# Optimization experiments

Hardware: AMD Instinct MI355X
Metric: run time of the kernel (lower is better)

The kernel has to match this reference:

```python
import jax, jax.numpy as jnp
import numpy as np

N_USER = 27094
M_SPOT = 42852
N_EDGE = 2_000_000
D_FEAT = 128


def setup_inputs() -> dict:
    key = jax.random.key(0)
    k1, k2, k3, k4 = jax.random.split(key, 4)
    spot_x = jax.random.normal(k1, (M_SPOT, D_FEAT), dtype=jnp.float32)
    user_x = jax.random.normal(k2, (N_USER, D_FEAT), dtype=jnp.float32)
    u_idx = jax.random.randint(k3, (N_EDGE,), 0, N_USER, dtype=jnp.int32)
    s_idx = jax.random.randint(k4, (N_EDGE,), 0, M_SPOT, dtype=jnp.int32)
    user_spot = jnp.stack([u_idx, s_idx], axis=0)  # [2, E]
    return {"spot_x": spot_x, "user_x": user_x, "user_spot": user_spot}


def reference(spot_x, user_x, user_spot):
    u = user_spot[0]  # [E] user index per edge
    s = user_spot[1]  # [E] spot index per edge
    # symmetric GCN normalization: 1/sqrt(deg_u * deg_s) per edge
    user_deg = jnp.bincount(u, length=N_USER)
    spot_deg = jnp.bincount(s, length=M_SPOT)
    div = jnp.sqrt((user_deg[u] * spot_deg[s]).astype(spot_x.dtype))[:, None]  # [E,1]
    # spot -> user aggregation
    source_spot = spot_x[s] / div                                   # [E, D]
    user_out = jax.ops.segment_sum(source_spot, u, num_segments=N_USER)
    # user -> spot aggregation
    source_user = user_x[u] / div                                   # [E, D]
    spot_out = jax.ops.segment_sum(source_user, s, num_segments=M_SPOT)
    return (spot_out, user_out)
```

## Files before the change

kernel.cpp:

```cpp
#include <hip/hip_runtime.h>
#include <stdint.h>


#define NPB_LOG2 6
#define NPB 64
#define MAXB 768
#define PART_CHUNK 2048
#define BH_CHUNK 16384
#define SORT_CAP 8192
#define CSCAN_CH 256

__device__ __forceinline__ ushort f2bf(float f) {
    uint32_t u = __float_as_uint(f);
    return (ushort)((u + 0x7fffu + ((u >> 16) & 1u)) >> 16);
}

__global__ __launch_bounds__(256) void bhist_kernel(
        const int* __restrict__ u, const int* __restrict__ s, int E,
        int nbu, int nbs, int* __restrict__ bd) {
    __shared__ int hist[2 * MAXB];
    const int tid = threadIdx.x;
    const int nb = nbu + nbs;
    const int beg = blockIdx.x * BH_CHUNK;
    const int end = min(beg + BH_CHUNK, E);
    for (int b = tid; b < nb; b += 256) hist[b] = 0;
    __syncthreads();
    for (int i = beg + tid; i < end; i += 256) {
        atomicAdd(&hist[u[i] >> NPB_LOG2], 1);
        atomicAdd(&hist[nbu + (s[i] >> NPB_LOG2)], 1);
    }
    __syncthreads();
    for (int b = tid; b < nb; b += 256) {
        int h = hist[b];
        if (h) atomicAdd(&bd[b], h);
    }
}

__global__ __launch_bounds__(1024) void scan2_kernel(
        const int* __restrict__ bd, int nbu, int nbs,
        int* __restrict__ buoff, int* __restrict__ bsoff,
        int* __restrict__ gcu, int* __restrict__ gcs) {
    __shared__ int wsums[16];
    __shared__ int total;
    const int tid = threadIdx.x, lane = tid & 63, wid = tid >> 6;
    const int n   = blockIdx.x ? nbs : nbu;
    const int* in = blockIdx.x ? (bd + nbu) : bd;
    int* out = blockIdx.x ? bsoff : buoff;
    int* gc  = blockIdx.x ? gcs   : gcu;
    int v = (tid < n) ? in[tid] : 0;
    int x = v;
#pragma unroll
    for (int d = 1; d < 64; d <<= 1) {
        int t = __shfl_up(x, d);
        if (lane >= d) x += t;
    }
    if (lane == 63) wsums[wid] = x;
    __syncthreads();
    if (tid == 0) {
        int run = 0;
#pragma unroll
        for (int w = 0; w < 16; ++w) { int t = wsums[w]; wsums[w] = run; run += t; }
        total = run;
    }
    __syncthreads();
    int excl = wsums[wid] + (x - v);
    if (tid < n) { out[tid] = excl; gc[tid] = excl; }
    if (tid == 0) out[n] = total;
}

__global__ void convert_kernel(const float* __restrict__ x, const float* __restrict__ isd,
                               ushort* __restrict__ xb, int n_rows) {
    int idx = blockIdx.x * blockDim.x + threadIdx.x;
    if (idx >= (n_rows << 6)) return;
    int row = idx >> 6, c = idx & 63;
    float w = isd[row];
    const float* xr = x + ((size_t)row << 7);
    ushort2 o;
    o.x = f2bf(xr[c] * w);
    o.y = f2bf(xr[c + 64] * w);
    *reinterpret_cast<ushort2*>(xb + ((size_t)row << 7) + 2 * c) = o;
}

__global__ __launch_bounds__(256) void part_kernel(
        const int* __restrict__ prim, const int* __restrict__ sec, int E,
        int nb, int* __restrict__ gcur, uint32_t* __restrict__ out) {
    __shared__ int hist[MAXB];
    __shared__ int loff[MAXB];
    __shared__ int gbase[MAXB];
    __shared__ int cur[MAXB];
    __shared__ int wsum[4];
    __shared__ uint32_t sbuf[PART_CHUNK];
    const int tid = threadIdx.x;
    const int lane = tid & 63;
    const int wid = tid >> 6;
    const int beg = blockIdx.x * PART_CHUNK;
    const int end = min(beg + PART_CHUNK, E);
    const int cnt_total = end - beg;
    for (int b = tid; b < nb; b += 256) hist[b] = 0;
    __syncthreads();
    for (int i = beg + tid; i < end; i += 256)
        atomicAdd(&hist[prim[i] >> NPB_LOG2], 1);
    __syncthreads();
    {
        int b0 = tid * 3;
        int h0 = (b0 + 0 < nb) ? hist[b0 + 0] : 0;
        int h1 = (b0 + 1 < nb) ? hist[b0 + 1] : 0;
        int h2 = (b0 + 2 < nb) ? hist[b0 + 2] : 0;
        int tsum = h0 + h1 + h2;
        int x = tsum;
#pragma unroll
        for (int d = 1; d < 64; d <<= 1) {
            int t = __shfl_up(x, d);
            if (lane >= d) x += t;
        }
        if (lane == 63) wsum[wid] = x;
        __syncthreads();
        if (tid == 0) {
            int run = 0;
#pragma unroll
            for (int w = 0; w < 4; ++w) { int t = wsum[w]; wsum[w] = run; run += t; }
        }
        __syncthreads();
        int base = wsum[wid] + (x - tsum);
        if (b0 + 0 < nb) loff[b0 + 0] = base;
        if (b0 + 1 < nb) loff[b0 + 1] = base + h0;
        if (b0 + 2 < nb) loff[b0 + 2] = base + h0 + h1;
    }
    __syncthreads();
    for (int b = tid; b < nb; b += 256) {
        cur[b] = loff[b];
        int c = hist[b];
        gbase[b] = c > 0 ? atomicAdd(&gcur[b], c) : 0;
    }
    __syncthreads();
    for (int i = beg + tid; i < end; i += 256) {
        int p = prim[i], s = sec[i];
        int b = p >> NPB_LOG2;
        int l = atomicAdd(&cur[b], 1);
        sbuf[l] = ((uint32_t)p << 16) | (uint32_t)s;
    }
    __syncthreads();
    for (int k = tid; k < cnt_total; k += 256) {
        uint32_t p = sbuf[k];
        int b = (int)(p >> (16 + NPB_LOG2));
        out[gbase[b] + (k - loff[b])] = p;
    }
}

__global__ __launch_bounds__(256) void bsort3_kernel(
        uint32_t* __restrict__ buf, const int* __restrict__ boff,
        float* __restrict__ isd, int n_rows) {
    __shared__ uint32_t stage[SORT_CAP];
    __shared__ int hist[NPB];
    __shared__ int cur[NPB];
    const int tid = threadIdx.x;
    const int jbeg = boff[blockIdx.x];
    const int cnt = boff[blockIdx.x + 1] - jbeg;
    const bool fits = (cnt <= SORT_CAP);
    if (tid < NPB) hist[tid] = 0;
    __syncthreads();
    for (int k = tid; k < cnt; k += 256) {
        uint32_t p = buf[jbeg + k];
        if (fits) stage[k] = p;
        atomicAdd(&hist[(p >> 16) & (NPB - 1)], 1);
    }
    __syncthreads();
    if (tid < NPB) {
        int h = hist[tid];
        int x = h;
#pragma unroll
        for (int d = 1; d < 64; d <<= 1) {
            int t = __shfl_up(x, d);
            if (tid >= d) x += t;
        }
        cur[tid] = x - h;
        int node = (blockIdx.x << NPB_LOG2) + tid;
        if (node < n_rows) isd[node] = h > 0 ? rsqrtf((float)h) : 0.f;
    }
    __syncthreads();
    if (fits) {
        for (int k = tid; k < cnt; k += 256) {
            uint32_t p = stage[k];
            int slot = atomicAdd(&cur[(p >> 16) & (NPB - 1)], 1);
            buf[jbeg + slot] = p;
        }
    }
}

__global__ __launch_bounds__(256) void cscan_kernel(
        const ushort* __restrict__ xb, const uint32_t* __restrict__ packed, int E,
        const float* __restrict__ isd, float* __restrict__ out) {
    const int lane = threadIdx.x & 63;
    const int wave = (blockIdx.x << 2) + (threadIdx.x >> 6);
    const int base = wave * CSCAN_CH;
    if (base >= E) return;
    const int n = min(CSCAN_CH, E - base);
    const uint32_t* pp = packed + base;
    float ax = 0.f, ay = 0.f;
    int cur = (int)(pp[0] >> 16);

#define ROW(pv) (*reinterpret_cast<const uint32_t*>( \
        xb + (((size_t)((pv) & 0xffffu)) << 7) + (lane << 1)))
#define UPX(rv) __uint_as_float((rv) << 16)
#define UPY(rv) __uint_as_float((rv) & 0xffff0000u)
#define FLUSH() do { float w_ = isd[cur];                                  \
        unsafeAtomicAdd(out + ((size_t)cur << 7) + lane, ax * w_);         \
        unsafeAtomicAdd(out + ((size_t)cur << 7) + 64 + lane, ay * w_);    \
        ax = 0.f; ay = 0.f; } while (0)
#define PROC(pv, rv) do { int d_ = (int)((pv) >> 16);                      \
        if (d_ != cur) { FLUSH(); cur = d_; }                              \
        ax += UPX(rv); ay += UPY(rv); } while (0)
#define GRP8(Aa, Ab, r0, r1, r2, r3, r4, r5, r6, r7) do {                  \
    if ((((Aa.x ^ Ab.w) >> 16) == 0) && ((int)(Aa.x >> 16) == cur)) {      \
        float sx = ((UPX(r0) + UPX(r1)) + (UPX(r2) + UPX(r3)))             \
                 + ((UPX(r4) + UPX(r5)) + (UPX(r6) + UPX(r7)));            \
        float sy = ((UPY(r0) + UPY(r1)) + (UPY(r2) + UPY(r3)))             \
                 + ((UPY(r4) + UPY(r5)) + (UPY(r6) + UPY(r7)));            \
        ax += sx; ay += sy;                                                \
    } else {                                                               \
        PROC(Aa.x, r0); PROC(Aa.y, r1); PROC(Aa.z, r2); PROC(Aa.w, r3);    \
        PROC(Ab.x, r4); PROC(Ab.y, r5); PROC(Ab.z, r6); PROC(Ab.w, r7);    \
    } } while (0)

    int k = 0;
    if (n >= 24) {
        uint4 P0a = *(const uint4*)(pp + 0),  P0b = *(const uint4*)(pp + 4);
        uint4 P1a = *(const uint4*)(pp + 8),  P1b = *(const uint4*)(pp + 12);
        uint32_t a0 = ROW(P0a.x), a1 = ROW(P0a.y), a2 = ROW(P0a.z), a3 = ROW(P0a.w),
                 a4 = ROW(P0b.x), a5 = ROW(P0b.y), a6 = ROW(P0b.z), a7 = ROW(P0b.w);
        uint4 P2a = *(const uint4*)(pp + 16), P2b = *(const uint4*)(pp + 20);
        uint32_t b0 = ROW(P1a.x), b1 = ROW(P1a.y), b2 = ROW(P1a.z), b3 = ROW(P1a.w),
                 b4 = ROW(P1b.x), b5 = ROW(P1b.y), b6 = ROW(P1b.z), b7 = ROW(P1b.w);
        for (k = 24; k + 8 <= n; k += 8) {
            uint4 P3a = *(const uint4*)(pp + k), P3b = *(const uint4*)(pp + k + 4);
            uint32_t c0 = ROW(P2a.x), c1 = ROW(P2a.y), c2 = ROW(P2a.z), c3 = ROW(P2a.w),
                     c4 = ROW(P2b.x), c5 = ROW(P2b.y), c6 = ROW(P2b.z), c7 = ROW(P2b.w);
            GRP8(P0a, P0b, a0, a1, a2, a3, a4, a5, a6, a7);
            P0a = P1a; P0b = P1b; P1a = P2a; P1b = P2b; P2a = P3a; P2b = P3b;
            a0 = b0; a1 = b1; a2 = b2; a3 = b3; a4 = b4; a5 = b5; a6 = b6; a7 = b7;
            b0 = c0; b1 = c1; b2 = c2; b3 = c3; b4 = c4; b5 = c5; b6 = c6; b7 = c7;
        }
        uint32_t c0 = ROW(P2a.x), c1 = ROW(P2a.y), c2 = ROW(P2a.z), c3 = ROW(P2a.w),
                 c4 = ROW(P2b.x), c5 = ROW(P2b.y), c6 = ROW(P2b.z), c7 = ROW(P2b.w);
        GRP8(P0a, P0b, a0, a1, a2, a3, a4, a5, a6, a7);
        GRP8(P1a, P1b, b0, b1, b2, b3, b4, b5, b6, b7);
        GRP8(P2a, P2b, c0, c1, c2, c3, c4, c5, c6, c7);
    }
    for (; k < n; ++k) {
        uint32_t p = pp[k];
        uint32_t r = ROW(p);
        PROC(p, r);
    }
    FLUSH();
#undef GRP8
#undef PROC
#undef FLUSH
#undef UPY
#undef UPX
#undef ROW
}


__global__ __launch_bounds__(1024) void scan_kernel(const int* __restrict__ in,
                                                    int* __restrict__ out, int n) {
    __shared__ int ws[17];
    const int tid  = threadIdx.x;
    const int lane = tid & 63;
    const int wid  = tid >> 6;
    int carry = 0;
    for (int base = 0; base < n; base += 4096) {
        int idx = base + tid * 4;
        int v0 = (idx + 0 < n) ? in[idx + 0] : 0;
        int v1 = (idx + 1 < n) ? in[idx + 1] : 0;
        int v2 = (idx + 2 < n) ? in[idx + 2] : 0;
        int v3 = (idx + 3 < n) ? in[idx + 3] : 0;
        int tsum = v0 + v1 + v2 + v3;
        int x = tsum;
#pragma unroll
        for (int d = 1; d < 64; d <<= 1) {
            int t = __shfl_up(x, d);
            if (lane >= d) x += t;
        }
        if (lane == 63) ws[wid] = x;
        __syncthreads();
        if (tid == 0) {
            int run = carry;
#pragma unroll
            for (int w = 0; w < 16; ++w) { int t = ws[w]; ws[w] = run; run += t; }
            carry = run;
        }
        __syncthreads();
        int excl = ws[wid] + (x - tsum);
        if (idx + 0 < n) out[idx + 0] = excl; excl += v0;
        if (idx + 1 < n) out[idx + 1] = excl; excl += v1;
        if (idx + 2 < n) out[idx + 2] = excl; excl += v2;
        if (idx + 3 < n) out[idx + 3] = excl;
        __syncthreads();
    }
    if (tid == 0) out[n] = carry;
}

__global__ void deg_kernel(const int* __restrict__ u, const int* __restrict__ s,
                           int E, int* __restrict__ udeg, int* __restrict__ sdeg) {
    int i = blockIdx.x * blockDim.x + threadIdx.x;
    int i4 = i * 4;
    if (i4 + 3 < E) {
        int4 a = *reinterpret_cast<const int4*>(u + i4);
        int4 b = *reinterpret_cast<const int4*>(s + i4);
        atomicAdd(&udeg[a.x], 1); atomicAdd(&udeg[a.y], 1);
        atomicAdd(&udeg[a.z], 1); atomicAdd(&udeg[a.w], 1);
        atomicAdd(&sdeg[b.x], 1); atomicAdd(&sdeg[b.y], 1);
        atomicAdd(&sdeg[b.z], 1); atomicAdd(&sdeg[b.w], 1);
    } else {
        for (int k = i4; k < E; ++k) {
            atomicAdd(&udeg[u[k]], 1);
            atomicAdd(&sdeg[s[k]], 1);
        }
    }
}

__global__ void init_isd_kernel(const int* __restrict__ udeg, const int* __restrict__ sdeg,
                                float* __restrict__ isd_u, float* __restrict__ isd_s,
                                int n_user, int m_spot) {
    int i = blockIdx.x * blockDim.x + threadIdx.x;
    if (i < n_user) { int d = udeg[i]; isd_u[i] = d > 0 ? rsqrtf((float)d) : 0.f; }
    if (i < m_spot) { int d = sdeg[i]; isd_s[i] = d > 0 ? rsqrtf((float)d) : 0.f; }
}

__global__ void breduce_kernel(const int* __restrict__ udeg, const int* __restrict__ sdeg,
                               int N, int M, int nbu, int nbs,
                               int* __restrict__ bdu, int* __restrict__ bds) {
    const int w = (blockIdx.x * blockDim.x + threadIdx.x) >> 6;
    const int lane = threadIdx.x & 63;
    if (w >= nbu + nbs) return;
    int v;
    if (w < nbu) {
        int i = (w << NPB_LOG2) + lane;
        v = (i < N) ? udeg[i] : 0;
    } else {
        int i = ((w - nbu) << NPB_LOG2) + lane;
        v = (i < M) ? sdeg[i] : 0;
    }
#pragma unroll
    for (int d = 32; d >= 1; d >>= 1) v += __shfl_down(v, d);
    if (lane == 0) {
        if (w < nbu) bdu[w] = v; else bds[w - nbu] = v;
    }
}

__global__ void gcur3_init_kernel(const int* __restrict__ buoff, const int* __restrict__ bsoff,
                                  int* __restrict__ gcu, int* __restrict__ gcs,
                                  int nbu, int nbs) {
    int i = blockIdx.x * blockDim.x + threadIdx.x;
    if (i < nbu) gcu[i] = buoff[i];
    if (i < nbs) gcs[i] = bsoff[i];
}

__global__ void gcur_init_kernel(const int* __restrict__ uoff, const int* __restrict__ soff,
                                 int* __restrict__ gcur_u, int* __restrict__ gcur_s,
                                 int nbu, int nbs) {
    int i = blockIdx.x * blockDim.x + threadIdx.x;
    if (i < nbu) gcur_u[i] = uoff[i << NPB_LOG2];
    if (i < nbs) gcur_s[i] = soff[i << NPB_LOG2];
}

__global__ __launch_bounds__(256) void bsort_kernel(
        const uint32_t* __restrict__ packed, const int* __restrict__ noff,
        int nodes, int* __restrict__ csr) {
    __shared__ int cur[NPB];
    const int tid = threadIdx.x;
    const int ubase = blockIdx.x << NPB_LOG2;
    const int nin = min(NPB, nodes - ubase);
    if (tid < nin) cur[tid] = noff[ubase + tid];
    __syncthreads();
    const int jbeg = noff[ubase];
    const int jend = noff[ubase + nin];
    for (int j = jbeg + tid; j < jend; j += 256) {
        uint32_t p = packed[j];
        int local = (int)(p >> 16) - ubase;
        int slot = atomicAdd(&cur[local], 1);
        csr[slot] = (int)(p & 0xffffu);
    }
}

__global__ __launch_bounds__(256) void gather_kernel(const float* __restrict__ x_src,
                                                     const int* __restrict__ nbr,
                                                     const int* __restrict__ off,
                                                     const float* __restrict__ isd_dst,
                                                     const float* __restrict__ isd_src,
                                                     float* __restrict__ out, int n_rows) {
    const int lane = threadIdx.x & 63;
    const int row  = blockIdx.x * 4 + (threadIdx.x >> 6);
    if (row >= n_rows) return;
    const int jbeg = off[row];
    const int jend = off[row + 1];
    const float wd = isd_dst[row];
    float ax = 0.f, ay = 0.f;
    if (jbeg < jend) {
        int sidx = nbr[jbeg];
        for (int j = jbeg; j < jend; ++j) {
            int snext = (j + 1 < jend) ? nbr[j + 1] : 0;
            float w = wd * isd_src[sidx];
            const float2 v = *reinterpret_cast<const float2*>(x_src + (size_t)sidx * 128 + lane * 2);
            ax = fmaf(v.x, w, ax);
            ay = fmaf(v.y, w, ay);
            sidx = snext;
        }
    }
    float2 r; r.x = ax; r.y = ay;
    *reinterpret_cast<float2*>(out + (size_t)row * 128 + lane * 2) = r;
}

__global__ __launch_bounds__(256) void scatter_kernel(const float* __restrict__ spot_x,
                                                      const float* __restrict__ user_x,
                                                      const int* __restrict__ u,
                                                      const int* __restrict__ s, int E,
                                                      const float* __restrict__ isd_u,
                                                      const float* __restrict__ isd_s,
                                                      float* __restrict__ spot_out,
                                                      float* __restrict__ user_out) {
    const int lane = threadIdx.x & 63;
    const int e = blockIdx.x * 4 + (threadIdx.x >> 6);
    if (e >= E) return;
    const int uu = u[e], ss = s[e];
    const float w = isd_u[uu] * isd_s[ss];
    const float2 sv = *reinterpret_cast<const float2*>(spot_x + (size_t)ss * 128 + lane * 2);
    const float2 uv = *reinterpret_cast<const float2*>(user_x + (size_t)uu * 128 + lane * 2);
    atomicAdd(&user_out[(size_t)uu * 128 + lane * 2 + 0], sv.x * w);
    atomicAdd(&user_out[(size_t)uu * 128 + lane * 2 + 1], sv.y * w);
    atomicAdd(&spot_out[(size_t)ss * 128 + lane * 2 + 0], uv.x * w);
    atomicAdd(&spot_out[(size_t)ss * 128 + lane * 2 + 1], uv.y * w);
}

static inline char* align256(char* p) {
    return (char*)(((uintptr_t)p + 255u) & ~(uintptr_t)255u);
}

extern "C" void kernel_launch(void* const* d_in, const int* in_sizes, int n_in,
                              void* d_out, int out_size, void* d_ws, size_t ws_size,
                              hipStream_t stream) {
    const float* spot_x = (const float*)d_in[0];
    const float* user_x = (const float*)d_in[1];
    const int*   edges  = (const int*)d_in[2];
    const int M = in_sizes[0] / 128;
    const int N = in_sizes[1] / 128;
    const int E = in_sizes[2] / 2;
    const int* u = edges;
    const int* s = edges + E;
    float* spot_out = (float*)d_out;
    float* user_out = (float*)d_out + (size_t)M * 128;

    const int nbu = (N + NPB - 1) / NPB;
    const int nbs = (M + NPB - 1) / NPB;
    const int nm = (N > M) ? N : M;
    const int gpart = (E + PART_CHUNK - 1) / PART_CHUNK;
    const int gscan = ((E + CSCAN_CH - 1) / CSCAN_CH + 3) / 4;

    {
        char* ws = (char*)d_ws;
        float*    isd_u = (float*)ws; ws = align256(ws + sizeof(float) * (size_t)N);
        float*    isd_s = (float*)ws; ws = align256(ws + sizeof(float) * (size_t)M);
        int*      bd    = (int*)ws;   ws = align256(ws + sizeof(int) * (size_t)(nbu + nbs));
        int*      buoff = (int*)ws;   ws = align256(ws + sizeof(int) * (size_t)(nbu + 1));
        int*      bsoff = (int*)ws;   ws = align256(ws + sizeof(int) * (size_t)(nbs + 1));
        int*      gcu   = (int*)ws;   ws = align256(ws + sizeof(int) * (size_t)nbu);
        int*      gcs   = (int*)ws;   ws = align256(ws + sizeof(int) * (size_t)nbs);
        uint32_t* bufU  = (uint32_t*)ws; ws = align256(ws + sizeof(uint32_t) * (size_t)E);
        uint32_t* bufS  = (uint32_t*)ws; ws = align256(ws + sizeof(uint32_t) * (size_t)E);
        ushort*   xb    = (ushort*)ws;
        size_t fast_needed = (size_t)(ws - (char*)d_ws) + sizeof(ushort) * ((size_t)nm * 128);

        if (fast_needed <= ws_size && nbu <= MAXB && nbs <= MAXB) {
            hipMemsetAsync(bd, 0, sizeof(int) * (size_t)(nbu + nbs), stream);
            hipMemsetAsync(d_out, 0, sizeof(float) * (size_t)out_size, stream);
            bhist_kernel<<<(E + BH_CHUNK - 1) / BH_CHUNK, 256, 0, stream>>>(
                u, s, E, nbu, nbs, bd);
            scan2_kernel<<<2, 1024, 0, stream>>>(bd, nbu, nbs, buoff, bsoff, gcu, gcs);
            part_kernel<<<gpart, 256, 0, stream>>>(u, s, E, nbu, gcu, bufU);
            part_kernel<<<gpart, 256, 0, stream>>>(s, u, E, nbs, gcs, bufS);
            bsort3_kernel<<<nbu, 256, 0, stream>>>(bufU, buoff, isd_u, N);
            bsort3_kernel<<<nbs, 256, 0, stream>>>(bufS, bsoff, isd_s, M);
            convert_kernel<<<((M << 6) + 255) / 256, 256, 0, stream>>>(spot_x, isd_s, xb, M);
            cscan_kernel<<<gscan, 256, 0, stream>>>(xb, bufU, E, isd_u, user_out);
            convert_kernel<<<((N << 6) + 255) / 256, 256, 0, stream>>>(user_x, isd_u, xb, N);
            cscan_kernel<<<gscan, 256, 0, stream>>>(xb, bufS, E, isd_s, spot_out);
            return;
        }
    }

    char* ws = (char*)d_ws;
    int*      udeg  = (int*)ws;  ws = align256(ws + sizeof(int) * (size_t)(N + M));
    int*      sdeg  = udeg + N;
    float*    isd_u = (float*)ws; ws = align256(ws + sizeof(float) * (size_t)N);
    float*    isd_s = (float*)ws; ws = align256(ws + sizeof(float) * (size_t)M);
    size_t fallback_needed = (size_t)(ws - (char*)d_ws);
    int*      uoff  = (int*)ws;  ws = align256(ws + sizeof(int) * (size_t)(N + 1));
    int*      soff  = (int*)ws;  ws = align256(ws + sizeof(int) * (size_t)(M + 1));
    int*      bdu   = (int*)ws;  ws = align256(ws + sizeof(int) * (size_t)nbu);
    int*      bds   = (int*)ws;  ws = align256(ws + sizeof(int) * (size_t)nbs);
    int*      buoff = (int*)ws;  ws = align256(ws + sizeof(int) * (size_t)(nbu + 1));
    int*      bsoff = (int*)ws;  ws = align256(ws + sizeof(int) * (size_t)(nbs + 1));
    int*      gcu   = (int*)ws;  ws = align256(ws + sizeof(int) * (size_t)nbu);
    int*      gcs   = (int*)ws;  ws = align256(ws + sizeof(int) * (size_t)nbs);
    uint32_t* bufA  = (uint32_t*)ws; ws = align256(ws + sizeof(uint32_t) * (size_t)E);
    char* mark = ws;
    ushort*   xbs   = (ushort*)mark;
    ushort*   xbu   = (ushort*)align256(mark + sizeof(ushort) * ((size_t)M * 128));
    size_t new_needed = (size_t)((char*)xbu - (char*)d_ws) + sizeof(ushort) * ((size_t)N * 128);
    int*      bufB  = (int*)mark;
    size_t old_needed = (size_t)(mark - (char*)d_ws) + sizeof(int) * (size_t)E;

    hipMemsetAsync(udeg, 0, sizeof(int) * (size_t)(N + M), stream);
    deg_kernel<<<(E / 4 + 255) / 256, 256, 0, stream>>>(u, s, E, udeg, sdeg);
    init_isd_kernel<<<(nm + 255) / 256, 256, 0, stream>>>(udeg, sdeg, isd_u, isd_s, N, M);

    if (new_needed <= ws_size && nbu <= MAXB && nbs <= MAXB) {
        convert_kernel<<<((M << 6) + 255) / 256, 256, 0, stream>>>(spot_x, isd_s, xbs, M);
        convert_kernel<<<((N << 6) + 255) / 256, 256, 0, stream>>>(user_x, isd_u, xbu, N);
        breduce_kernel<<<((nbu + nbs) * 64 + 255) / 256, 256, 0, stream>>>(
            udeg, sdeg, N, M, nbu, nbs, bdu, bds);
        scan_kernel<<<1, 1024, 0, stream>>>(bdu, buoff, nbu);
        scan_kernel<<<1, 1024, 0, stream>>>(bds, bsoff, nbs);
        gcur3_init_kernel<<<(nbs + nbu + 255) / 256, 256, 0, stream>>>(
            buoff, bsoff, gcu, gcs, nbu, nbs);
        hipMemsetAsync(d_out, 0, sizeof(float) * (size_t)out_size, stream);
        part_kernel<<<gpart, 256, 0, stream>>>(u, s, E, nbu, gcu, bufA);
        bsort3_kernel<<<nbu, 256, 0, stream>>>(bufA, buoff, isd_u, N);
        cscan_kernel<<<gscan, 256, 0, stream>>>(xbs, bufA, E, isd_u, user_out);
        part_kernel<<<gpart, 256, 0, stream>>>(s, u, E, nbs, gcs, bufA);
        bsort3_kernel<<<nbs, 256, 0, stream>>>(bufA, bsoff, isd_s, M);
        cscan_kernel<<<gscan, 256, 0, stream>>>(xbu, bufA, E, isd_s, spot_out);
    } else if (old_needed <= ws_size && nbu <= MAXB && nbs <= MAXB) {
        scan_kernel<<<1, 1024, 0, stream>>>(udeg, uoff, N);
        scan_kernel<<<1, 1024, 0, stream>>>(sdeg, soff, M);
        gcur_init_kernel<<<(nbs + nbu + 255) / 256, 256, 0, stream>>>(uoff, soff, gcu, gcs, nbu, nbs);
        part_kernel<<<gpart, 256, 0, stream>>>(u, s, E, nbu, gcu, bufA);
        bsort_kernel<<<nbu, 256, 0, stream>>>(bufA, uoff, N, bufB);
        gather_kernel<<<(N + 3) / 4, 256, 0, stream>>>(spot_x, bufB, uoff,
                                                       isd_u, isd_s, user_out, N);
        part_kernel<<<gpart, 256, 0, stream>>>(s, u, E, nbs, gcs, bufA);
        bsort_kernel<<<nbs, 256, 0, stream>>>(bufA, soff, M, bufB);
        gather_kernel<<<(M + 3) / 4, 256, 0, stream>>>(user_x, bufB, soff,
                                                       isd_s, isd_u, spot_out, M);
    } else if (fallback_needed <= ws_size) {
        hipMemsetAsync(d_out, 0, sizeof(float) * (size_t)out_size, stream);
        scatter_kernel<<<((size_t)E + 3) / 4, 256, 0, stream>>>(spot_x, user_x, u, s, E,
                                                                isd_u, isd_s, spot_out, user_out);
    }
}
```

Baseline: 270.4 us.

## Fuse per-bucket sort into segmented scan kernel using shared-memory staging

Replaces the separate bucket-sort and chunked scan kernels with a fused kernel that sorts each 64-node bucket into shared memory and then has 8 waves scan slices of that sorted list, flushing atomically per destination node. A lightweight degree-only kernel computes spot normalization ahead of the first conversion, since the fused kernel only yields the destination degrees. This removes the global write-back of sorted buffers and one kernel launch per direction, and reads inverse degrees from shared memory. In exchange, work per block follows bucket size, so load may be uneven, and the software pipeline is shallower than the previous three-stage prefetch.

Measured after the change: 274.9 us. No clear change (+1.7%).

```diff
diff --git a/kernel.cpp b/kernel.cpp
--- a/kernel.cpp
+++ b/kernel.cpp
@@ -147,23 +147,50 @@
     }
 }
 
-__global__ __launch_bounds__(256) void bsort3_kernel(
-        uint32_t* __restrict__ buf, const int* __restrict__ boff,
+__global__ __launch_bounds__(256) void bdeg_kernel(
+        const uint32_t* __restrict__ buf, const int* __restrict__ boff,
         float* __restrict__ isd, int n_rows) {
-    __shared__ uint32_t stage[SORT_CAP];
     __shared__ int hist[NPB];
-    __shared__ int cur[NPB];
     const int tid = threadIdx.x;
     const int jbeg = boff[blockIdx.x];
     const int cnt = boff[blockIdx.x + 1] - jbeg;
+    if (tid < NPB) hist[tid] = 0;
+    __syncthreads();
+    for (int k = tid; k < cnt; k += 256)
+        atomicAdd(&hist[(buf[jbeg + k] >> 16) & (NPB - 1)], 1);
+    __syncthreads();
+    if (tid < NPB) {
+        int node = (blockIdx.x << NPB_LOG2) + tid;
+        if (node < n_rows) {
+            int h = hist[tid];
+            isd[node] = h > 0 ? rsqrtf((float)h) : 0.f;
+        }
+    }
+}
+
+__global__ __launch_bounds__(512) void fscan_kernel(
+        const ushort* __restrict__ xb, const uint32_t* __restrict__ buf,
+        const int* __restrict__ boff, float* __restrict__ isd_out,
+        float* __restrict__ out, int n_rows) {
+    __shared__ uint32_t sorted[SORT_CAP];
+    __shared__ int hist[NPB];
+    __shared__ int scur[NPB];
+    __shared__ float isdl[NPB];
+    const int tid = threadIdx.x;
+    const int jbeg = boff[blockIdx.x];
+    const int cnt = boff[blockIdx.x + 1] - jbeg;
+    if (cnt <= 0) {
+        if (tid < NPB) {
+            int node = (blockIdx.x << NPB_LOG2) + tid;
+            if (node < n_rows) isd_out[node] = 0.f;
+        }
+        return;
+    }
     const bool fits = (cnt <= SORT_CAP);
     if (tid < NPB) hist[tid] = 0;
     __syncthreads();
-    for (int k = tid; k < cnt; k += 256) {
-        uint32_t p = buf[jbeg + k];
-        if (fits) stage[k] = p;
-        atomicAdd(&hist[(p >> 16) & (NPB - 1)], 1);
-    }
+    for (int k = tid; k < cnt; k += 512)
+        atomicAdd(&hist[(buf[jbeg + k] >> 16) & (NPB - 1)], 1);
     __syncthreads();
     if (tid < NPB) {
         int h = hist[tid];
@@ -173,81 +200,75 @@
             int t = __shfl_up(x, d);
             if (tid >= d) x += t;
         }
-        cur[tid] = x - h;
+        scur[tid] = x - h;
+        float iv = h > 0 ? rsqrtf((float)h) : 0.f;
+        isdl[tid] = iv;
         int node = (blockIdx.x << NPB_LOG2) + tid;
-        if (node < n_rows) isd[node] = h > 0 ? rsqrtf((float)h) : 0.f;
+        if (node < n_rows) isd_out[node] = iv;
     }
     __syncthreads();
     if (fits) {
-        for (int k = tid; k < cnt; k += 256) {
-            uint32_t p = stage[k];
-            int slot = atomicAdd(&cur[(p >> 16) & (NPB - 1)], 1);
-            buf[jbeg + slot] = p;
-        }
-    }
-}
-
-__global__ __launch_bounds__(256) void cscan_kernel(
-        const ushort* __restrict__ xb, const uint32_t* __restrict__ packed, int E,
-        const float* __restrict__ isd, float* __restrict__ out) {
-    const int lane = threadIdx.x & 63;
-    const int wave = (blockIdx.x << 2) + (threadIdx.x >> 6);
-    const int base = wave * CSCAN_CH;
-    if (base >= E) return;
-    const int n = min(CSCAN_CH, E - base);
-    const uint32_t* pp = packed + base;
-    float ax = 0.f, ay = 0.f;
-    int cur = (int)(pp[0] >> 16);
-
+        for (int k = tid; k < cnt; k += 512) {
+            uint32_t p = buf[jbeg + k];
+            int slot = atomicAdd(&scur[(p >> 16) & (NPB - 1)], 1);
+            sorted[slot] = p;
+        }
+    }
+    __syncthreads();
+    const int wid = tid >> 6, lane = tid & 63;
+    const int cs = (cnt + 7) >> 3;
+    const int beg = wid * cs;
+    const int end = min(beg + cs, cnt);
+    if (beg >= end) return;
+    const int n = end - beg;
+
+#define QLD(i) (fits ? sorted[i] : buf[jbeg + (i)])
 #define ROW(pv) (*reinterpret_cast<const uint32_t*>( \
         xb + (((size_t)((pv) & 0xffffu)) << 7) + (lane << 1)))
 #define UPX(rv) __uint_as_float((rv) << 16)
 #define UPY(rv) __uint_as_float((rv) & 0xffff0000u)
-#define FLUSH() do { float w_ = isd[cur];                                  \
-        unsafeAtomicAdd(out + ((size_t)cur << 7) + lane, ax * w_);         \
-        unsafeAtomicAdd(out + ((size_t)cur << 7) + 64 + lane, ay * w_);    \
+#define FLUSH() do { float w_ = isdl[curd & (NPB - 1)];                    \
+        unsafeAtomicAdd(out + ((size_t)curd << 7) + lane, ax * w_);        \
+        unsafeAtomicAdd(out + ((size_t)curd << 7) + 64 + lane, ay * w_);   \
         ax = 0.f; ay = 0.f; } while (0)
 #define PROC(pv, rv) do { int d_ = (int)((pv) >> 16);                      \
-        if (d_ != cur) { FLUSH(); cur = d_; }                              \
+        if (d_ != curd) { FLUSH(); curd = d_; }                            \
         ax += UPX(rv); ay += UPY(rv); } while (0)
-#define GRP8(Aa, Ab, r0, r1, r2, r3, r4, r5, r6, r7) do {                  \
-    if ((((Aa.x ^ Ab.w) >> 16) == 0) && ((int)(Aa.x >> 16) == cur)) {      \
+#define GRP8(q0,q1,q2,q3,q4,q5,q6,q7, r0,r1,r2,r3,r4,r5,r6,r7) do {        \
+    if ((((q0 ^ q7) >> 16) == 0) && ((int)(q0 >> 16) == curd)) {           \
         float sx = ((UPX(r0) + UPX(r1)) + (UPX(r2) + UPX(r3)))             \
                  + ((UPX(r4) + UPX(r5)) + (UPX(r6) + UPX(r7)));            \
         float sy = ((UPY(r0) + UPY(r1)) + (UPY(r2) + UPY(r3)))             \
                  + ((UPY(r4) + UPY(r5)) + (UPY(r6) + UPY(r7)));            \
         ax += sx; ay += sy;                                                \
     } else {                                                               \
-        PROC(Aa.x, r0); PROC(Aa.y, r1); PROC(Aa.z, r2); PROC(Aa.w, r3);    \
-        PROC(Ab.x, r4); PROC(Ab.y, r5); PROC(Ab.z, r6); PROC(Ab.w, r7);    \
+        PROC(q0, r0); PROC(q1, r1); PROC(q2, r2); PROC(q3, r3);            \
+        PROC(q4, r4); PROC(q5, r5); PROC(q6, r6); PROC(q7, r7);            \
     } } while (0)
 
+    float ax = 0.f, ay = 0.f;
+    int curd = (int)(QLD(beg) >> 16);
     int k = 0;
-    if (n >= 24) {
-        uint4 P0a = *(const uint4*)(pp + 0),  P0b = *(const uint4*)(pp + 4);
-        uint4 P1a = *(const uint4*)(pp + 8),  P1b = *(const uint4*)(pp + 12);
-        uint32_t a0 = ROW(P0a.x), a1 = ROW(P0a.y), a2 = ROW(P0a.z), a3 = ROW(P0a.w),
-                 a4 = ROW(P0b.x), a5 = ROW(P0b.y), a6 = ROW(P0b.z), a7 = ROW(P0b.w);
-        uint4 P2a = *(const uint4*)(pp + 16), P2b = *(const uint4*)(pp + 20);
-        uint32_t b0 = ROW(P1a.x), b1 = ROW(P1a.y), b2 = ROW(P1a.z), b3 = ROW(P1a.w),
-                 b4 = ROW(P1b.x), b5 = ROW(P1b.y), b6 = ROW(P1b.z), b7 = ROW(P1b.w);
-        for (k = 24; k + 8 <= n; k += 8) {
-            uint4 P3a = *(const uint4*)(pp + k), P3b = *(const uint4*)(pp + k + 4);
-            uint32_t c0 = ROW(P2a.x), c1 = ROW(P2a.y), c2 = ROW(P2a.z), c3 = ROW(P2a.w),
-                     c4 = ROW(P2b.x), c5 = ROW(P2b.y), c6 = ROW(P2b.z), c7 = ROW(P2b.w);
-            GRP8(P0a, P0b, a0, a1, a2, a3, a4, a5, a6, a7);
-            P0a = P1a; P0b = P1b; P1a = P2a; P1b = P2b; P2a = P3a; P2b = P3b;
+    if (n >= 16) {
+        uint32_t a0 = QLD(beg + 0), a1 = QLD(beg + 1), a2 = QLD(beg + 2), a3 = QLD(beg + 3),
+                 a4 = QLD(beg + 4), a5 = QLD(beg + 5), a6 = QLD(beg + 6), a7 = QLD(beg + 7);
+        uint32_t r0 = ROW(a0), r1 = ROW(a1), r2 = ROW(a2), r3 = ROW(a3),
+                 r4 = ROW(a4), r5 = ROW(a5), r6 = ROW(a6), r7 = ROW(a7);
+        for (k = 8; k + 8 <= n; k += 8) {
+            uint32_t b0 = QLD(beg + k + 0), b1 = QLD(beg + k + 1),
+                     b2 = QLD(beg + k + 2), b3 = QLD(beg + k + 3),
+                     b4 = QLD(beg + k + 4), b5 = QLD(beg + k + 5),
+                     b6 = QLD(beg + k + 6), b7 = QLD(beg + k + 7);
+            uint32_t s0 = ROW(b0), s1 = ROW(b1), s2 = ROW(b2), s3 = ROW(b3),
+                     s4 = ROW(b4), s5 = ROW(b5), s6 = ROW(b6), s7 = ROW(b7);
+            GRP8(a0,a1,a2,a3,a4,a5,a6,a7, r0,r1,r2,r3,r4,r5,r6,r7);
             a0 = b0; a1 = b1; a2 = b2; a3 = b3; a4 = b4; a5 = b5; a6 = b6; a7 = b7;
-            b0 = c0; b1 = c1; b2 = c2; b3 = c3; b4 = c4; b5 = c5; b6 = c6; b7 = c7;
-        }
-        uint32_t c0 = ROW(P2a.x), c1 = ROW(P2a.y), c2 = ROW(P2a.z), c3 = ROW(P2a.w),
-                 c4 = ROW(P2b.x), c5 = ROW(P2b.y), c6 = ROW(P2b.z), c7 = ROW(P2b.w);
-        GRP8(P0a, P0b, a0, a1, a2, a3, a4, a5, a6, a7);
-        GRP8(P1a, P1b, b0, b1, b2, b3, b4, b5, b6, b7);
-        GRP8(P2a, P2b, c0, c1, c2, c3, c4, c5, c6, c7);
+            r0 = s0; r1 = s1; r2 = s2; r3 = s3; r4 = s4; r5 = s5; r6 = s6; r7 = s7;
+        }
+        GRP8(a0,a1,a2,a3,a4,a5,a6,a7, r0,r1,r2,r3,r4,r5,r6,r7);
     }
     for (; k < n; ++k) {
-        uint32_t p = pp[k];
+        uint32_t p = QLD(beg + k);
         uint32_t r = ROW(p);
         PROC(p, r);
     }
@@ -258,6 +279,7 @@
 #undef UPY
 #undef UPX
 #undef ROW
+#undef QLD
 }
 
 
@@ -381,6 +403,102 @@
         int slot = atomicAdd(&cur[local], 1);
         csr[slot] = (int)(p & 0xffffu);
     }
+}
+
+__global__ __launch_bounds__(256) void bsort3_kernel(
+        uint32_t* __restrict__ buf, const int* __restrict__ boff,
+        float* __restrict__ isd, int n_rows) {
+    __shared__ uint32_t stage[SORT_CAP];
+    __shared__ int hist[NPB];
+    __shared__ int cur[NPB];
+    const int tid = threadIdx.x;
+    const int jbeg = boff[blockIdx.x];
+    const int cnt = boff[blockIdx.x + 1] - jbeg;
+    const bool fits = (cnt <= SORT_CAP);
+    if (tid < NPB) hist[tid] = 0;
+    __syncthreads();
+    for (int k = tid; k < cnt; k += 256) {
+        uint32_t p = buf[jbeg + k];
+        if (fits) stage[k] = p;
+        atomicAdd(&hist[(p >> 16) & (NPB - 1)], 1);
+    }
+    __syncthreads();
+    if (tid < NPB) {
+        int h = hist[tid];
+        int x = h;
+#pragma unroll
+        for (int d = 1; d < 64; d <<= 1) {
+            int t = __shfl_up(x, d);
+            if (tid >= d) x += t;
+        }
+        cur[tid] = x - h;
+        int node = (blockIdx.x << NPB_LOG2) + tid;
+        if (node < n_rows) isd[node] = h > 0 ? rsqrtf((float)h) : 0.f;
+    }
+    __syncthreads();
+    if (fits) {
+        for (int k = tid; k < cnt; k += 256) {
+            uint32_t p = stage[k];
+            int slot = atomicAdd(&cur[(p >> 16) & (NPB - 1)], 1);
+            buf[jbeg + slot] = p;
+        }
+    }
+}
+
+__global__ __launch_bounds__(256) void cscan_kernel(
+        const ushort* __restrict__ xb, const uint32_t* __restrict__ packed, int E,
+        const float* __restrict__ isd, float* __restrict__ out) {
+    const int lane = threadIdx.x & 63;
+    const int wave = (blockIdx.x << 2) + (threadIdx.x >> 6);
+    const int base = wave * CSCAN_CH;
+    if (base >= E) return;
+    const int n = min(CSCAN_CH, E - base);
+    const uint32_t* pp = packed + base;
+    float ax = 0.f, ay = 0.f;
+    int cur = (int)(pp[0] >> 16);
+
+#define ROW(pv) (*reinterpret_cast<const uint32_t*>( \
+        xb + (((size_t)((pv) & 0xffffu)) << 7) + (lane << 1)))
+#define PROC(pv, rv) do {                                                  \
+        int d_ = (int)((pv) >> 16);                                        \
+        if (d_ != cur) {                                                   \
+            float w_ = isd[cur];                                           \
+            unsafeAtomicAdd(out + ((size_t)cur << 7) + lane, ax * w_);     \
+            unsafeAtomicAdd(out + ((size_t)cur << 7) + 64 + lane, ay * w_);\
+            ax = 0.f; ay = 0.f; cur = d_;                                  \
+        }                                                                  \
+        ax += __uint_as_float((rv) << 16);                                 \
+        ay += __uint_as_float((rv) & 0xffff0000u);                         \
+    } while (0)
+
+    int k = 0;
+    if (n >= 16) {
+        uint4 Pa = *reinterpret_cast<const uint4*>(pp);
+        uint4 Pb = *reinterpret_cast<const uint4*>(pp + 4);
+        uint32_t r0 = ROW(Pa.x), r1 = ROW(Pa.y), r2 = ROW(Pa.z), r3 = ROW(Pa.w);
+        uint32_t r4 = ROW(Pb.x), r5 = ROW(Pb.y), r6 = ROW(Pb.z), r7 = ROW(Pb.w);
+        for (k = 8; k + 8 <= n; k += 8) {
+            uint4 Na = *reinterpret_cast<const uint4*>(pp + k);
+            uint4 Nb = *reinterpret_cast<const uint4*>(pp + k + 4);
+            PROC(Pa.x, r0); PROC(Pa.y, r1); PROC(Pa.z, r2); PROC(Pa.w, r3);
+            PROC(Pb.x, r4); PROC(Pb.y, r5); PROC(Pb.z, r6); PROC(Pb.w, r7);
+            r0 = ROW(Na.x); r1 = ROW(Na.y); r2 = ROW(Na.z); r3 = ROW(Na.w);
+            r4 = ROW(Nb.x); r5 = ROW(Nb.y); r6 = ROW(Nb.z); r7 = ROW(Nb.w);
+            Pa = Na; Pb = Nb;
+        }
+        PROC(Pa.x, r0); PROC(Pa.y, r1); PROC(Pa.z, r2); PROC(Pa.w, r3);
+        PROC(Pb.x, r4); PROC(Pb.y, r5); PROC(Pb.z, r6); PROC(Pb.w, r7);
+    }
+    for (; k < n; ++k) {
+        uint32_t p = pp[k];
+        uint32_t r = ROW(p);
+        PROC(p, r);
+    }
+    float w = isd[cur];
+    unsafeAtomicAdd(out + ((size_t)cur << 7) + lane, ax * w);
+    unsafeAtomicAdd(out + ((size_t)cur << 7) + 64 + lane, ay * w);
+#undef PROC
+#undef ROW
 }
 
 __global__ __launch_bounds__(256) void gather_kernel(const float* __restrict__ x_src,
@@ -478,12 +596,11 @@
             scan2_kernel<<<2, 1024, 0, stream>>>(bd, nbu, nbs, buoff, bsoff, gcu, gcs);
             part_kernel<<<gpart, 256, 0, stream>>>(u, s, E, nbu, gcu, bufU);
             part_kernel<<<gpart, 256, 0, stream>>>(s, u, E, nbs, gcs, bufS);
-            bsort3_kernel<<<nbu, 256, 0, stream>>>(bufU, buoff, isd_u, N);
-            bsort3_kernel<<<nbs, 256, 0, stream>>>(bufS, bsoff, isd_s, M);
+            bdeg_kernel<<<nbs, 256, 0, stream>>>(bufS, bsoff, isd_s, M);
             convert_kernel<<<((M << 6) + 255) / 256, 256, 0, stream>>>(spot_x, isd_s, xb, M);
-            cscan_kernel<<<gscan, 256, 0, stream>>>(xb, bufU, E, isd_u, user_out);
+            fscan_kernel<<<nbu, 512, 0, stream>>>(xb, bufU, buoff, isd_u, user_out, N);
             convert_kernel<<<((N << 6) + 255) / 256, 256, 0, stream>>>(user_x, isd_u, xb, N);
-            cscan_kernel<<<gscan, 256, 0, stream>>>(xb, bufS, E, isd_s, spot_out);
+            fscan_kernel<<<nbs, 512, 0, stream>>>(xb, bufS, bsoff, isd_s, spot_out, M);
             return;
         }
     }
```
